# Kernel optimization log

Hardware: AMD Instinct MI355X
Metric: run time of the kernel (lower is better)

The kernel has to match this reference:

```python
import jax, jax.numpy as jnp
import numpy as np

SOFTMAX_SCALE = 1.0  # module default

def setup_inputs() -> dict:
    key = jax.random.key(0)
    ks = jax.random.split(key, 5)
    B, H, S, D = 2, 8, 192, 64
    shp = (B, H, S, D)
    return {
        "q":  jax.random.normal(ks[0], shp, dtype=jnp.float32),
        "k1": jax.random.normal(ks[1], shp, dtype=jnp.float32),
        "k2": jax.random.normal(ks[2], shp, dtype=jnp.float32),
        "v1": jax.random.normal(ks[3], shp, dtype=jnp.float32),
        "v2": jax.random.normal(ks[4], shp, dtype=jnp.float32),
    }

def reference(q, k1, k2, v1, v2):
    B, H, S, D = q.shape
    # trilinear scores: torch einsum 'bnth,bnsh,bnqh->bntsq' then rearrange to [b,n,q,(t s)]
    # equivalently compute [b,n,q,t,s] directly
    scores = jnp.einsum('bnth,bnsh,bnqh->bnqts', k1, k2, q)  # [B,H,S,S,S]
    flat = scores.reshape(B, H, S, S * S) * SOFTMAX_SCALE
    m = jnp.max(flat, axis=-1, keepdims=True)               # [B,H,S,1]
    p = jnp.exp(flat - m)
    suma = jnp.sum(p, axis=-1, keepdims=True)
    attn = (p / suma).reshape(B, H, S, S, S)                # [B,H,q,t,s]
    z = jnp.einsum('bnqts,bntd->bnqd', attn, v1) + jnp.einsum('bnqts,bnsd->bnqd', attn, v2)
    lse = m[..., 0] + jnp.log(suma[..., 0])                 # [B,H,S]
    return (z, lse)
```

## Files before the change

kernel.cpp:

```cpp
#include <hip/hip_runtime.h>
#include <hip/hip_bf16.h>
#include <math.h>


#define SS 192
#define DD 64
#define NT 512

typedef __attribute__((ext_vector_type(8))) short bf16x8;
typedef __attribute__((ext_vector_type(4))) float f32x4;

static __device__ __forceinline__ unsigned pk_bf16(float a, float b) {
    union { __hip_bfloat162 h; unsigned u; } cv;
    cv.h = __float22bfloat162_rn(float2{a, b});
    return cv.u;
}

#define DPP_STEP(v, CTRL)                                                   \
    (v) += __int_as_float(__builtin_amdgcn_update_dpp(                      \
        0, __float_as_int(v), (CTRL), 0xF, 0xF, true))

static __device__ __forceinline__ float row16_sum(float v) {
    DPP_STEP(v, 0xB1);
    DPP_STEP(v, 0x4E);
    DPP_STEP(v, 0x141);
    DPP_STEP(v, 0x140);
    return v;
}

__global__ __launch_bounds__(256) void k2_pack(const float* __restrict__ k2g,
                                               uint4* __restrict__ outp) {
    int i = blockIdx.x * 256 + threadIdx.x;
    const float4* in = (const float4*)k2g;
    float4 a = in[2 * i], b = in[2 * i + 1];
    uint4 w;
    w.x = pk_bf16(a.x, a.y);
    w.y = pk_bf16(a.z, a.w);
    w.z = pk_bf16(b.x, b.y);
    w.w = pk_bf16(b.z, b.w);
    int ih = i & 1535;
    int r = ih >> 3, c = ih & 7;
    outp[(i & ~1535) | (r * 8 + (c ^ (r & 7)))] = w;
}

__launch_bounds__(NT, 4)
__global__ void tritt_fwd(const float* __restrict__ qg,
                          const float* __restrict__ k1g,
                          const uint4* __restrict__ k2p,
                          const float* __restrict__ v1g,
                          const float* __restrict__ v2g,
                          float* __restrict__ zg,
                          float* __restrict__ lseg) {
    __shared__ uint4 k2l[SS * 8];
    __shared__ uint4 wl[SS * 8];
    __shared__ float At[SS];
    __shared__ float As[SS];
    __shared__ float zsh[DD];

    const int tid = threadIdx.x;
    const int bid = blockIdx.x;
    const int head = bid / SS;
    const size_t hb = (size_t)head * SS * DD;

    const uint4* k2h = k2p + (size_t)head * (SS * 8);
    #pragma unroll
    for (int it = 0; it < (SS * 8) / NT; ++it) {
        int f8 = tid + it * NT;
        __builtin_amdgcn_global_load_lds(
            (const __attribute__((address_space(1))) unsigned int*)(k2h + f8),
            (__attribute__((address_space(3))) unsigned int*)&k2l[f8],
            16, 0, 0);
    }

    if (tid < SS) At[tid] = 0.f;
    else if (tid < 2 * SS) As[tid - SS] = 0.f;
    else if (tid < 2 * SS + DD) zsh[tid - 2 * SS] = 0.f;

    const float L2E = 1.44269504088896340736f;
    const float4* k1v = (const float4*)(k1g + hb);
    const float4* qv  = (const float4*)(qg + (size_t)bid * DD);
    {
        const int c = tid & 7;
        float4 q0 = qv[2 * c], q1 = qv[2 * c + 1];
        q0.x *= L2E; q0.y *= L2E; q0.z *= L2E; q0.w *= L2E;
        q1.x *= L2E; q1.y *= L2E; q1.z *= L2E; q1.w *= L2E;
        #pragma unroll
        for (int it = 0; it < (SS * 8) / NT; ++it) {
            int f8 = tid + it * NT;
            int r = f8 >> 3;
            float4 a0 = k1v[2 * f8], a1 = k1v[2 * f8 + 1];
            uint4 w;
            w.x = pk_bf16(a0.x * q0.x, a0.y * q0.y);
            w.y = pk_bf16(a0.z * q0.z, a0.w * q0.w);
            w.z = pk_bf16(a1.x * q1.x, a1.y * q1.y);
            w.w = pk_bf16(a1.z * q1.z, a1.w * q1.w);
            wl[r * 8 + (c ^ (r & 7))] = w;
        }
    }
    __syncthreads();

    const int lane = tid & 63;
    const int wid  = tid >> 6;
    const int wt   = wid >> 2;
    const int ws   = wid & 3;
    const int lrow = lane & 15;
    const int lk   = lane >> 4;
    const int lrm  = lrow & 7;

    const int sw0 = lk ^ lrm;
    const int sw1 = (4 + lk) ^ lrm;
    const int ab  = (wt * 96 + lrow) * 8;
    const int bb  = (ws * 48 + lrow) * 8;

    float colp[3] = {0.f, 0.f, 0.f};
    #pragma unroll
    for (int i = 0; i < 6; ++i) {
        bf16x8 afr0 = *(const bf16x8*)&wl[ab + i * 128 + sw0];
        bf16x8 afr1 = *(const bf16x8*)&wl[ab + i * 128 + sw1];
        float rs[4] = {0.f, 0.f, 0.f, 0.f};
        #pragma unroll
        for (int j = 0; j < 3; ++j) {
            f32x4 acc = (f32x4){0.f, 0.f, 0.f, 0.f};
            bf16x8 b0 = *(const bf16x8*)&k2l[bb + j * 128 + sw0];
            acc = __builtin_amdgcn_mfma_f32_16x16x32_bf16(afr0, b0, acc, 0, 0, 0);
            bf16x8 b1 = *(const bf16x8*)&k2l[bb + j * 128 + sw1];
            acc = __builtin_amdgcn_mfma_f32_16x16x32_bf16(afr1, b1, acc, 0, 0, 0);
            #pragma unroll
            for (int r = 0; r < 4; ++r) {
                float p = __builtin_amdgcn_exp2f(acc[r]);
                rs[r] += p;
                colp[j] += p;
            }
        }
        #pragma unroll
        for (int r = 0; r < 4; ++r) {
            float v = row16_sum(rs[r]);
            if (lrow == 0)
                atomicAdd(&At[wt * 96 + i * 16 + lk * 4 + r], v);
        }
    }
    #pragma unroll
    for (int j = 0; j < 3; ++j) {
        float v = colp[j];
        v += __shfl_xor(v, 16, 64);
        v += __shfl_xor(v, 32, 64);
        if (lane < 16)
            atomicAdd(&As[ws * 48 + j * 16 + lane], v);
    }
    __syncthreads();

    float suma = At[lane] + At[lane + 64] + At[lane + 128];
    suma = row16_sum(suma);
    suma += __shfl_xor(suma, 16, 64);
    suma += __shfl_xor(suma, 32, 64);

    const int d = tid & 63;
    const int g = tid >> 6;
    const float* v1p = v1g + hb;
    const float* v2p = v2g + hb;
    float zp = 0.f;
    #pragma unroll 4
    for (int r = 0; r < 24; ++r) {
        int t = g * 24 + r;
        zp = fmaf(At[t], v1p[t * DD + d], zp);
        zp = fmaf(As[t], v2p[t * DD + d], zp);
    }
    atomicAdd(&zsh[d], zp);
    __syncthreads();

    if (tid < DD) zg[(size_t)bid * DD + tid] = zsh[tid] / suma;
    if (tid == 0) lseg[bid] = logf(suma);
}

extern "C" void kernel_launch(void* const* d_in, const int* in_sizes, int n_in,
                              void* d_out, int out_size, void* d_ws, size_t ws_size,
                              hipStream_t stream) {
    const float* q  = (const float*)d_in[0];
    const float* k1 = (const float*)d_in[1];
    const float* k2 = (const float*)d_in[2];
    const float* v1 = (const float*)d_in[3];
    const float* v2 = (const float*)d_in[4];
    float* out = (float*)d_out;

    const int nq = in_sizes[0] / DD;
    const int nheads = nq / SS;
    float* zout   = out;
    float* lseout = out + (size_t)nq * DD;
    uint4* k2pack = (uint4*)d_ws;

    int n8 = nheads * SS * DD / 8;
    hipLaunchKernelGGL(k2_pack, dim3(n8 / 256), dim3(256), 0, stream, k2, k2pack);

    dim3 grid(nq), block(NT);
    hipLaunchKernelGGL(tritt_fwd, grid, block, 0, stream,
                       q, k1, (const uint4*)k2pack, v1, v2, zout, lseout);
}
```

Before: 59.09 us.

## Cut register pressure: roll loops, per-tile column atomics, raise occupancy bound

Raises the launch-bounds minimum blocks per CU from 4 to 8 and switches the score loops to `#pragma unroll 1`, so the compiler must keep register use low and more wavefronts can be resident. The column partial sums are now reduced and atomically added to shared memory after every 16x16 tile, which removes the per-thread colp array but issues more LDS atomics and shuffles. The pack kernel uses 512-thread blocks. Rolled loops give up instruction-level parallelism between the MFMA and exp chains, and the extra atomics add LDS traffic.

```diff
diff --git a/kernel.cpp b/kernel.cpp
--- a/kernel.cpp
+++ b/kernel.cpp
@@ -28,9 +28,9 @@
     return v;
 }
 
-__global__ __launch_bounds__(256) void k2_pack(const float* __restrict__ k2g,
+__global__ __launch_bounds__(512) void k2_pack(const float* __restrict__ k2g,
                                                uint4* __restrict__ outp) {
-    int i = blockIdx.x * 256 + threadIdx.x;
+    int i = blockIdx.x * 512 + threadIdx.x;
     const float4* in = (const float4*)k2g;
     float4 a = in[2 * i], b = in[2 * i + 1];
     uint4 w;
@@ -43,7 +43,7 @@
     outp[(i & ~1535) | (r * 8 + (c ^ (r & 7)))] = w;
 }
 
-__launch_bounds__(NT, 4)
+__launch_bounds__(NT, 8)
 __global__ void tritt_fwd(const float* __restrict__ qg,
                           const float* __restrict__ k1g,
                           const uint4* __restrict__ k2p,
@@ -81,19 +81,19 @@
     const float4* qv  = (const float4*)(qg + (size_t)bid * DD);
     {
         const int c = tid & 7;
-        float4 q0 = qv[2 * c], q1 = qv[2 * c + 1];
-        q0.x *= L2E; q0.y *= L2E; q0.z *= L2E; q0.w *= L2E;
-        q1.x *= L2E; q1.y *= L2E; q1.z *= L2E; q1.w *= L2E;
-        #pragma unroll
+        float4 p0 = qv[2 * c], p1 = qv[2 * c + 1];
+        p0.x *= L2E; p0.y *= L2E; p0.z *= L2E; p0.w *= L2E;
+        p1.x *= L2E; p1.y *= L2E; p1.z *= L2E; p1.w *= L2E;
+        #pragma unroll 1
         for (int it = 0; it < (SS * 8) / NT; ++it) {
             int f8 = tid + it * NT;
             int r = f8 >> 3;
             float4 a0 = k1v[2 * f8], a1 = k1v[2 * f8 + 1];
             uint4 w;
-            w.x = pk_bf16(a0.x * q0.x, a0.y * q0.y);
-            w.y = pk_bf16(a0.z * q0.z, a0.w * q0.w);
-            w.z = pk_bf16(a1.x * q1.x, a1.y * q1.y);
-            w.w = pk_bf16(a1.z * q1.z, a1.w * q1.w);
+            w.x = pk_bf16(a0.x * p0.x, a0.y * p0.y);
+            w.y = pk_bf16(a0.z * p0.z, a0.w * p0.w);
+            w.z = pk_bf16(a1.x * p1.x, a1.y * p1.y);
+            w.w = pk_bf16(a1.z * p1.z, a1.w * p1.w);
             wl[r * 8 + (c ^ (r & 7))] = w;
         }
     }
@@ -112,40 +112,35 @@
     const int ab  = (wt * 96 + lrow) * 8;
     const int bb  = (ws * 48 + lrow) * 8;
 
-    float colp[3] = {0.f, 0.f, 0.f};
-    #pragma unroll
+    #pragma unroll 1
     for (int i = 0; i < 6; ++i) {
         bf16x8 afr0 = *(const bf16x8*)&wl[ab + i * 128 + sw0];
         bf16x8 afr1 = *(const bf16x8*)&wl[ab + i * 128 + sw1];
-        float rs[4] = {0.f, 0.f, 0.f, 0.f};
-        #pragma unroll
+        f32x4 rsv = (f32x4){0.f, 0.f, 0.f, 0.f};
+        #pragma unroll 1
         for (int j = 0; j < 3; ++j) {
             f32x4 acc = (f32x4){0.f, 0.f, 0.f, 0.f};
             bf16x8 b0 = *(const bf16x8*)&k2l[bb + j * 128 + sw0];
             acc = __builtin_amdgcn_mfma_f32_16x16x32_bf16(afr0, b0, acc, 0, 0, 0);
             bf16x8 b1 = *(const bf16x8*)&k2l[bb + j * 128 + sw1];
             acc = __builtin_amdgcn_mfma_f32_16x16x32_bf16(afr1, b1, acc, 0, 0, 0);
+            f32x4 pv;
             #pragma unroll
-            for (int r = 0; r < 4; ++r) {
-                float p = __builtin_amdgcn_exp2f(acc[r]);
-                rs[r] += p;
-                colp[j] += p;
-            }
+            for (int r = 0; r < 4; ++r)
+                pv[r] = __builtin_amdgcn_exp2f(acc[r]);
+            rsv += pv;
+            float cs = (pv[0] + pv[1]) + (pv[2] + pv[3]);
+            cs += __shfl_xor(cs, 16, 64);
+            cs += __shfl_xor(cs, 32, 64);
+            if (lane < 16)
+                atomicAdd(&As[ws * 48 + j * 16 + lane], cs);
         }
         #pragma unroll
         for (int r = 0; r < 4; ++r) {
-            float v = row16_sum(rs[r]);
+            float v = row16_sum(rsv[r]);
             if (lrow == 0)
                 atomicAdd(&At[wt * 96 + i * 16 + lk * 4 + r], v);
         }
-    }
-    #pragma unroll
-    for (int j = 0; j < 3; ++j) {
-        float v = colp[j];
-        v += __shfl_xor(v, 16, 64);
-        v += __shfl_xor(v, 32, 64);
-        if (lane < 16)
-            atomicAdd(&As[ws * 48 + j * 16 + lane], v);
     }
     __syncthreads();
 
@@ -154,8 +149,8 @@
     suma += __shfl_xor(suma, 16, 64);
     suma += __shfl_xor(suma, 32, 64);
 
-    const int d = tid & 63;
-    const int g = tid >> 6;
+    const int d = lane;
+    const int g = wid;
     const float* v1p = v1g + hb;
     const float* v2p = v2g + hb;
     float zp = 0.f;
@@ -189,7 +184,7 @@
     uint4* k2pack = (uint4*)d_ws;
 
     int n8 = nheads * SS * DD / 8;
-    hipLaunchKernelGGL(k2_pack, dim3(n8 / 256), dim3(256), 0, stream, k2, k2pack);
+    hipLaunchKernelGGL(k2_pack, dim3(n8 / 512), dim3(512), 0, stream, k2, k2pack);
 
     dim3 grid(nq), block(NT);
     hipLaunchKernelGGL(tritt_fwd, grid, block, 0, stream,
```

New measurement: 92.52 us. 1.57x slower.
